# Performance work log

Measured on AMD Instinct MI355X. Metric: run time of the kernel, lower is better.

The kernel has to match this reference:

```python
import jax, jax.numpy as jnp
import numpy as np

BETA = 0.5
ITEM_NUM = 100000
REGION_NUM = 1000
EMBED = 128
HIDDEN = 256
B, H = 1024, 256


def setup_inputs() -> dict:
    key = jax.random.key(0)
    ks = jax.random.split(key, 10)
    history = jax.random.randint(ks[0], (B, H), 0, ITEM_NUM)
    target = jax.random.randint(ks[1], (B,), 0, ITEM_NUM)
    history_region = jax.random.randint(ks[2], (B, H), 0, REGION_NUM)
    target_region = jax.random.randint(ks[3], (B,), 0, REGION_NUM)
    E_hist = 0.01 * jax.random.normal(ks[4], (ITEM_NUM, EMBED), dtype=jnp.float32)
    E_targ = 0.01 * jax.random.normal(ks[5], (ITEM_NUM, EMBED), dtype=jnp.float32)
    E_reg = 0.01 * jax.random.normal(ks[6], (REGION_NUM, EMBED), dtype=jnp.float32)
    lim1 = 1.0 / np.sqrt(2 * EMBED)
    W1 = jax.random.uniform(ks[7], (2 * EMBED, HIDDEN), jnp.float32, -lim1, lim1)
    b1 = jnp.zeros((HIDDEN,), jnp.float32)
    lim2 = 1.0 / np.sqrt(HIDDEN)
    w2 = jax.random.uniform(ks[8], (HIDDEN,), jnp.float32, -lim2, lim2)
    return {"history": history, "target": target,
            "history_region": history_region, "target_region": target_region,
            "E_hist": E_hist, "E_targ": E_targ, "E_reg": E_reg,
            "W1": W1, "b1": b1, "w2": w2}


def reference(history, target, history_region, target_region,
              E_hist, E_targ, E_reg, W1, b1, w2):
    # gathers + concat: hist [B,H,2d], tgt [B,2d]
    hist = jnp.concatenate([E_hist[history], E_reg[history_region]], axis=-1)
    tgt = jnp.concatenate([E_targ[target], E_reg[target_region]], axis=-1)
    # elementwise product broadcast over history dim
    inp = hist * tgt[:, None, :]                      # [B,H,2d]
    hid = jax.nn.relu(jnp.einsum('bhd,dk->bhk', inp, W1) + b1)
    scores = jnp.einsum('bhk,k->bh', hid, w2)         # [B,H]
    mask = (history != target[:, None]).astype(scores.dtype)
    exp_a = jnp.exp(scores) * mask                    # [B,H]
    denom = jnp.power(jnp.sum(exp_a, axis=-1), BETA)  # [B]
    attn = exp_a / denom[:, None]                     # [B,H]
    # weighted reduction: sum_h sum_d hist*attn*tgt
    pred = jnp.einsum('bhd,bh,bd->b', hist, attn, tgt)
    return jax.nn.sigmoid(pred)
```

## Files before the change

### kernel.cpp

```cpp
#include <hip/hip_runtime.h>
#include <hip/hip_bf16.h>

#define NB 1024
#define NH 256
#define EMB 128
#define TWOD 256
#define HID 256
#define ROWS 128
#define BPB 2
#define NBLK (NB * BPB)

typedef __attribute__((ext_vector_type(4))) float f32x4;
typedef __attribute__((ext_vector_type(8))) short bf16x8;

__device__ __forceinline__ unsigned short f2bf(float f) {
  union { float f; unsigned u; } v; v.f = f;
  unsigned u = v.u;
  unsigned r = (u + 0x7fffu + ((u >> 16) & 1u)) >> 16;
  return (unsigned short)r;
}

__global__ __launch_bounds__(256) void prep_w1t(const float* __restrict__ W1,
                                                unsigned short* __restrict__ W1T) {
  const int bx = blockIdx.x & 3;
  const int by = blockIdx.x >> 2;
  __shared__ float tile[64][65];
  const int tr = threadIdx.x >> 6;
  const int tc = threadIdx.x & 63;
  #pragma unroll
  for (int i = 0; i < 16; ++i) {
    const int d = bx * 64 + i * 4 + tr;
    tile[i * 4 + tr][tc] = W1[(size_t)d * HID + by * 64 + tc];
  }
  __syncthreads();
  #pragma unroll
  for (int i = 0; i < 16; ++i) {
    const int n = by * 64 + i * 4 + tr;
    W1T[(size_t)n * TWOD + bx * 64 + tc] = f2bf(tile[tc][i * 4 + tr]);
  }
}

__global__ __launch_bounds__(512, 4) void nais_main(
    const int* __restrict__ history, const int* __restrict__ target,
    const int* __restrict__ hregion, const int* __restrict__ tregion,
    const float* __restrict__ E_hist, const float* __restrict__ E_targ,
    const float* __restrict__ E_reg,
    const unsigned short* __restrict__ W1T, const float* __restrict__ b1,
    const float* __restrict__ w2,
    float* __restrict__ part_se, float* __restrict__ part_sd)
{
  const int blk = blockIdx.x;
  const int b = blk >> 1;
  const int r0 = (blk & 1) * ROWS;
  const int tid = threadIdx.x;
  const int lane = tid & 63;
  const int wave = tid >> 6;
  const int l15 = lane & 15;
  const int lhi = lane >> 4;
  const int l31 = lane & 31;
  const int halfsel = lane >> 5;

  __shared__ __align__(16) unsigned short inp_lds[ROWS * 256];
  __shared__ float dot_lds[ROWS];
  __shared__ int items_lds[ROWS];
  __shared__ float score_parts[8][ROWS];

  const float* tsrc = halfsel ? (E_reg + (size_t)tregion[b] * EMB)
                              : (E_targ + (size_t)target[b] * EMB);
  const f32x4 t = *(const f32x4*)(tsrc + l31 * 4);
  const int tgt_item = target[b];

  const int* keysrc = halfsel ? hregion : history;
  const float* table = halfsel ? E_reg : E_hist;

  {
    int key[16];
    #pragma unroll
    for (int s = 0; s < 16; ++s)
      key[s] = keysrc[b * NH + r0 + wave * 16 + s];

    #pragma unroll
    for (int pass = 0; pass < 2; ++pass) {
      f32x4 vb[8];
      #pragma unroll
      for (int s = 0; s < 8; ++s)
        vb[s] = *(const f32x4*)(table + (size_t)key[pass * 8 + s] * EMB + l31 * 4);

      #pragma unroll
      for (int s = 0; s < 8; ++s) {
        const int row = wave * 16 + pass * 8 + s;
        if (lane == 0) items_lds[row] = key[pass * 8 + s];
        f32x4 v = vb[s] * t;
        float ds = v[0] + v[1] + v[2] + v[3];
        ds += __shfl_xor(ds, 1);
        ds += __shfl_xor(ds, 2);
        ds += __shfl_xor(ds, 4);
        ds += __shfl_xor(ds, 8);
        ds += __shfl_xor(ds, 16);
        ds += __shfl_xor(ds, 32);
        if (lane == 0) dot_lds[row] = ds;

        float2 f01; f01.x = v[0]; f01.y = v[1];
        float2 f23; f23.x = v[2]; f23.y = v[3];
        __hip_bfloat162 p0 = __float22bfloat162_rn(f01);
        __hip_bfloat162 p1 = __float22bfloat162_rn(f23);
        union { __hip_bfloat162 h; unsigned u; } c0, c1;
        c0.h = p0; c1.h = p1;
        const int g = halfsel * 16 + (l31 >> 1);
        const int gs = g ^ (row & 7) ^ ((g >> 3) & 3);
        unsigned* dst = (unsigned*)&inp_lds[row * 256 + gs * 8 + (lane & 1) * 4];
        dst[0] = c0.u; dst[1] = c1.u;
      }
    }
  }
  __syncthreads();

  {
    const int col0 = wave * 32;
    float b1v[2], w2v[2];
    #pragma unroll
    for (int n = 0; n < 2; ++n) {
      const int colh = col0 + n * 16 + l15;
      b1v[n] = b1[colh];
      w2v[n] = w2[colh];
    }

    f32x4 acc[2][4][2];
    #pragma unroll
    for (int c = 0; c < 2; ++c)
      #pragma unroll
      for (int m = 0; m < 4; ++m)
        #pragma unroll
        for (int n = 0; n < 2; ++n)
          acc[c][m][n] = (f32x4){0.f, 0.f, 0.f, 0.f};

    #pragma unroll
    for (int kk = 0; kk < 8; ++kk) {
      bf16x8 bfr[2];
      #pragma unroll
      for (int n = 0; n < 2; ++n) {
        const int colh = col0 + n * 16 + l15;
        bfr[n] = *(const bf16x8*)(W1T + (size_t)colh * TWOD + kk * 32 + lhi * 8);
      }
      bf16x8 af[2][4];
      #pragma unroll
      for (int c = 0; c < 2; ++c)
        #pragma unroll
        for (int m = 0; m < 4; ++m) {
          const int row = c * 64 + m * 16 + l15;
          const int gk = kk * 4 + lhi;
          const int gs = gk ^ (row & 7) ^ ((gk >> 3) & 3);
          af[c][m] = *(const bf16x8*)(&inp_lds[row * 256 + gs * 8]);
        }
      __builtin_amdgcn_s_setprio(1);
      #pragma unroll
      for (int c = 0; c < 2; ++c)
        #pragma unroll
        for (int m = 0; m < 4; ++m)
          #pragma unroll
          for (int n = 0; n < 2; ++n)
            acc[c][m][n] = __builtin_amdgcn_mfma_f32_16x16x32_bf16(af[c][m], bfr[n], acc[c][m][n], 0, 0, 0);
      __builtin_amdgcn_s_setprio(0);
    }

    #pragma unroll
    for (int c = 0; c < 2; ++c) {
      #pragma unroll
      for (int m = 0; m < 4; ++m) {
        #pragma unroll
        for (int r = 0; r < 4; ++r) {
          float p = 0.f;
          #pragma unroll
          for (int n = 0; n < 2; ++n) {
            float hv = acc[c][m][n][r] + b1v[n];
            hv = hv > 0.f ? hv : 0.f;
            p += hv * w2v[n];
          }
          p += __shfl_xor(p, 1);
          p += __shfl_xor(p, 2);
          p += __shfl_xor(p, 4);
          p += __shfl_xor(p, 8);
          if (l15 == 0) score_parts[wave][c * 64 + m * 16 + lhi * 4 + r] = p;
        }
      }
    }
  }
  __syncthreads();

  if (wave < 2) {
    const int lrow = wave * 64 + lane;
    float sc = 0.f;
    #pragma unroll
    for (int w = 0; w < 8; ++w) sc += score_parts[w][lrow];
    float e = (items_lds[lrow] != tgt_item) ? expf(sc) : 0.f;
    float ed = e * dot_lds[lrow];
    #pragma unroll
    for (int off = 32; off >= 1; off >>= 1) {
      e += __shfl_xor(e, off);
      ed += __shfl_xor(ed, off);
    }
    if (lane == 0) {
      part_se[blk * 2 + wave] = e;
      part_sd[blk * 2 + wave] = ed;
    }
  }
}

__global__ __launch_bounds__(256) void finalize(const float* __restrict__ part_se,
                                                const float* __restrict__ part_sd,
                                                float* __restrict__ out) {
  const int b = blockIdx.x * 256 + threadIdx.x;
  if (b < NB) {
    float se = 0.f, sd = 0.f;
    #pragma unroll
    for (int i = 0; i < BPB * 2; ++i) {
      se += part_se[b * BPB * 2 + i];
      sd += part_sd[b * BPB * 2 + i];
    }
    const float pred = (se > 0.f) ? (sd / sqrtf(se)) : 0.f;
    out[b] = 1.f / (1.f + expf(-pred));
  }
}

extern "C" void kernel_launch(void* const* d_in, const int* in_sizes, int n_in,
                              void* d_out, int out_size, void* d_ws, size_t ws_size,
                              hipStream_t stream) {
  const int* history = (const int*)d_in[0];
  const int* target  = (const int*)d_in[1];
  const int* hregion = (const int*)d_in[2];
  const int* tregion = (const int*)d_in[3];
  const float* E_hist = (const float*)d_in[4];
  const float* E_targ = (const float*)d_in[5];
  const float* E_reg  = (const float*)d_in[6];
  const float* W1 = (const float*)d_in[7];
  const float* b1 = (const float*)d_in[8];
  const float* w2 = (const float*)d_in[9];
  float* out = (float*)d_out;

  char* p = (char*)d_ws;
  unsigned short* W1T = (unsigned short*)p;  p += (size_t)TWOD * HID * 2;
  float* part_se = (float*)p;                p += (size_t)NBLK * 2 * 4;
  float* part_sd = (float*)p;

  prep_w1t<<<16, 256, 0, stream>>>(W1, W1T);
  nais_main<<<NBLK, 512, 0, stream>>>(history, target, hregion, tregion,
                                      E_hist, E_targ, E_reg, W1T, b1, w2,
                                      part_se, part_sd);
  finalize<<<(NB + 255) / 256, 256, 0, stream>>>(part_se, part_sd, out);
}
```

Baseline: 87.48 us.

## Warp-specialize producer/consumer waves with double-buffered chunks, one block per batch row

Each block now handles a whole batch row in four 64-row chunks. Four waves gather embeddings into a double-buffered LDS tile while the other four run the MFMA GEMM on the previous chunk, so gather latency overlaps with compute. The softmax-style reduction and sigmoid are folded into the main kernel, which removes the partial-sum buffers and the finalize launch. In exchange only half the waves do MFMA work, and a block barrier is needed at every chunk step.

```diff
diff --git a/kernel.cpp b/kernel.cpp
--- a/kernel.cpp
+++ b/kernel.cpp
@@ -6,9 +6,8 @@
 #define EMB 128
 #define TWOD 256
 #define HID 256
-#define ROWS 128
-#define BPB 2
-#define NBLK (NB * BPB)
+#define CR 64
+#define NCH 4
 
 typedef __attribute__((ext_vector_type(4))) float f32x4;
 typedef __attribute__((ext_vector_type(8))) short bf16x8;
@@ -46,12 +45,9 @@
     const float* __restrict__ E_hist, const float* __restrict__ E_targ,
     const float* __restrict__ E_reg,
     const unsigned short* __restrict__ W1T, const float* __restrict__ b1,
-    const float* __restrict__ w2,
-    float* __restrict__ part_se, float* __restrict__ part_sd)
+    const float* __restrict__ w2, float* __restrict__ out)
 {
-  const int blk = blockIdx.x;
-  const int b = blk >> 1;
-  const int r0 = (blk & 1) * ROWS;
+  const int b = blockIdx.x;
   const int tid = threadIdx.x;
   const int lane = tid & 63;
   const int wave = tid >> 6;
@@ -60,36 +56,48 @@
   const int l31 = lane & 31;
   const int halfsel = lane >> 5;
 
-  __shared__ __align__(16) unsigned short inp_lds[ROWS * 256];
-  __shared__ float dot_lds[ROWS];
-  __shared__ int items_lds[ROWS];
-  __shared__ float score_parts[8][ROWS];
-
-  const float* tsrc = halfsel ? (E_reg + (size_t)tregion[b] * EMB)
-                              : (E_targ + (size_t)target[b] * EMB);
-  const f32x4 t = *(const f32x4*)(tsrc + l31 * 4);
+  __shared__ __align__(16) unsigned short inp[2][CR * 256];
+  __shared__ float score_parts[2][4][CR];
+  __shared__ float dot_lds[NCH][CR];
+  __shared__ int items_lds[NCH][CR];
+
   const int tgt_item = target[b];
 
-  const int* keysrc = halfsel ? hregion : history;
-  const float* table = halfsel ? E_reg : E_hist;
-
-  {
+  f32x4 t;
+  const int* keysrc = history;
+  const float* table = E_hist;
+  float b1v[4], w2v[4];
+
+  if (wave < 4) {
+    const float* tsrc = halfsel ? (E_reg + (size_t)tregion[b] * EMB)
+                                : (E_targ + (size_t)target[b] * EMB);
+    t = *(const f32x4*)(tsrc + l31 * 4);
+    keysrc = halfsel ? hregion : history;
+    table = halfsel ? E_reg : E_hist;
+  } else {
+    const int col0 = (wave - 4) * 64;
+    #pragma unroll
+    for (int n = 0; n < 4; ++n) {
+      b1v[n] = b1[col0 + n * 16 + l15];
+      w2v[n] = w2[col0 + n * 16 + l15];
+    }
+  }
+
+  auto FILL = [&](int c, int buf) {
     int key[16];
     #pragma unroll
     for (int s = 0; s < 16; ++s)
-      key[s] = keysrc[b * NH + r0 + wave * 16 + s];
-
+      key[s] = keysrc[b * NH + c * CR + wave * 16 + s];
     #pragma unroll
     for (int pass = 0; pass < 2; ++pass) {
       f32x4 vb[8];
       #pragma unroll
       for (int s = 0; s < 8; ++s)
         vb[s] = *(const f32x4*)(table + (size_t)key[pass * 8 + s] * EMB + l31 * 4);
-
       #pragma unroll
       for (int s = 0; s < 8; ++s) {
         const int row = wave * 16 + pass * 8 + s;
-        if (lane == 0) items_lds[row] = key[pass * 8 + s];
+        if (lane == 0) items_lds[c][row] = key[pass * 8 + s];
         f32x4 v = vb[s] * t;
         float ds = v[0] + v[1] + v[2] + v[3];
         ds += __shfl_xor(ds, 1);
@@ -98,127 +106,110 @@
         ds += __shfl_xor(ds, 8);
         ds += __shfl_xor(ds, 16);
         ds += __shfl_xor(ds, 32);
-        if (lane == 0) dot_lds[row] = ds;
-
+        if (lane == 0) dot_lds[c][row] = ds;
         float2 f01; f01.x = v[0]; f01.y = v[1];
         float2 f23; f23.x = v[2]; f23.y = v[3];
-        __hip_bfloat162 p0 = __float22bfloat162_rn(f01);
-        __hip_bfloat162 p1 = __float22bfloat162_rn(f23);
         union { __hip_bfloat162 h; unsigned u; } c0, c1;
-        c0.h = p0; c1.h = p1;
+        c0.h = __float22bfloat162_rn(f01);
+        c1.h = __float22bfloat162_rn(f23);
         const int g = halfsel * 16 + (l31 >> 1);
         const int gs = g ^ (row & 7) ^ ((g >> 3) & 3);
-        unsigned* dst = (unsigned*)&inp_lds[row * 256 + gs * 8 + (lane & 1) * 4];
+        unsigned* dst = (unsigned*)&inp[buf][row * 256 + gs * 8 + (lane & 1) * 4];
         dst[0] = c0.u; dst[1] = c1.u;
       }
     }
-  }
-  __syncthreads();
-
-  {
-    const int col0 = wave * 32;
-    float b1v[2], w2v[2];
-    #pragma unroll
-    for (int n = 0; n < 2; ++n) {
-      const int colh = col0 + n * 16 + l15;
-      b1v[n] = b1[colh];
-      w2v[n] = w2[colh];
-    }
-
-    f32x4 acc[2][4][2];
-    #pragma unroll
-    for (int c = 0; c < 2; ++c)
+  };
+
+  float acc_e = 0.f, acc_ed = 0.f;
+
+  auto P3 = [&](int c) {
+    const int par = c & 1;
+    const float sc = score_parts[par][0][lane] + score_parts[par][1][lane] +
+                     score_parts[par][2][lane] + score_parts[par][3][lane];
+    const float e = (items_lds[c][lane] != tgt_item) ? expf(sc) : 0.f;
+    acc_e += e;
+    acc_ed += e * dot_lds[c][lane];
+  };
+
+  auto GEMM = [&](int c, int buf) {
+    const int col0 = (wave - 4) * 64;
+    f32x4 acc[4][4];
+    #pragma unroll
+    for (int m = 0; m < 4; ++m)
+      #pragma unroll
+      for (int n = 0; n < 4; ++n)
+        acc[m][n] = (f32x4){0.f, 0.f, 0.f, 0.f};
+
+    #pragma unroll
+    for (int kk = 0; kk < 8; ++kk) {
+      bf16x8 bfr[4];
+      #pragma unroll
+      for (int n = 0; n < 4; ++n)
+        bfr[n] = *(const bf16x8*)(W1T + (size_t)(col0 + n * 16 + l15) * TWOD + kk * 32 + lhi * 8);
+      bf16x8 af[4];
+      #pragma unroll
+      for (int m = 0; m < 4; ++m) {
+        const int row = m * 16 + l15;
+        const int gk = kk * 4 + lhi;
+        const int gs = gk ^ (row & 7) ^ ((gk >> 3) & 3);
+        af[m] = *(const bf16x8*)(&inp[buf][row * 256 + gs * 8]);
+      }
+      __builtin_amdgcn_s_setprio(1);
       #pragma unroll
       for (int m = 0; m < 4; ++m)
         #pragma unroll
-        for (int n = 0; n < 2; ++n)
-          acc[c][m][n] = (f32x4){0.f, 0.f, 0.f, 0.f};
-
-    #pragma unroll
-    for (int kk = 0; kk < 8; ++kk) {
-      bf16x8 bfr[2];
-      #pragma unroll
-      for (int n = 0; n < 2; ++n) {
-        const int colh = col0 + n * 16 + l15;
-        bfr[n] = *(const bf16x8*)(W1T + (size_t)colh * TWOD + kk * 32 + lhi * 8);
+        for (int n = 0; n < 4; ++n)
+          acc[m][n] = __builtin_amdgcn_mfma_f32_16x16x32_bf16(af[m], bfr[n], acc[m][n], 0, 0, 0);
+      __builtin_amdgcn_s_setprio(0);
+    }
+
+    const int cw = wave - 4;
+    #pragma unroll
+    for (int m = 0; m < 4; ++m) {
+      #pragma unroll
+      for (int r = 0; r < 4; ++r) {
+        float p = 0.f;
+        #pragma unroll
+        for (int n = 0; n < 4; ++n) {
+          float hv = acc[m][n][r] + b1v[n];
+          hv = hv > 0.f ? hv : 0.f;
+          p += hv * w2v[n];
+        }
+        p += __shfl_xor(p, 1);
+        p += __shfl_xor(p, 2);
+        p += __shfl_xor(p, 4);
+        p += __shfl_xor(p, 8);
+        if (l15 == 0) score_parts[c & 1][cw][m * 16 + lhi * 4 + r] = p;
       }
-      bf16x8 af[2][4];
-      #pragma unroll
-      for (int c = 0; c < 2; ++c)
-        #pragma unroll
-        for (int m = 0; m < 4; ++m) {
-          const int row = c * 64 + m * 16 + l15;
-          const int gk = kk * 4 + lhi;
-          const int gs = gk ^ (row & 7) ^ ((gk >> 3) & 3);
-          af[c][m] = *(const bf16x8*)(&inp_lds[row * 256 + gs * 8]);
-        }
-      __builtin_amdgcn_s_setprio(1);
-      #pragma unroll
-      for (int c = 0; c < 2; ++c)
-        #pragma unroll
-        for (int m = 0; m < 4; ++m)
-          #pragma unroll
-          for (int n = 0; n < 2; ++n)
-            acc[c][m][n] = __builtin_amdgcn_mfma_f32_16x16x32_bf16(af[c][m], bfr[n], acc[c][m][n], 0, 0, 0);
-      __builtin_amdgcn_s_setprio(0);
-    }
-
-    #pragma unroll
-    for (int c = 0; c < 2; ++c) {
-      #pragma unroll
-      for (int m = 0; m < 4; ++m) {
-        #pragma unroll
-        for (int r = 0; r < 4; ++r) {
-          float p = 0.f;
-          #pragma unroll
-          for (int n = 0; n < 2; ++n) {
-            float hv = acc[c][m][n][r] + b1v[n];
-            hv = hv > 0.f ? hv : 0.f;
-            p += hv * w2v[n];
-          }
-          p += __shfl_xor(p, 1);
-          p += __shfl_xor(p, 2);
-          p += __shfl_xor(p, 4);
-          p += __shfl_xor(p, 8);
-          if (l15 == 0) score_parts[wave][c * 64 + m * 16 + lhi * 4 + r] = p;
-        }
-      }
-    }
-  }
+    }
+  };
+
+  if (wave < 4) FILL(0, 0);
   __syncthreads();
 
-  if (wave < 2) {
-    const int lrow = wave * 64 + lane;
-    float sc = 0.f;
-    #pragma unroll
-    for (int w = 0; w < 8; ++w) sc += score_parts[w][lrow];
-    float e = (items_lds[lrow] != tgt_item) ? expf(sc) : 0.f;
-    float ed = e * dot_lds[lrow];
+  #pragma unroll
+  for (int tt = 0; tt < NCH; ++tt) {
+    if (wave < 4) {
+      if (tt < NCH - 1) FILL(tt + 1, (tt + 1) & 1);
+      if (wave == 0 && tt >= 1) P3(tt - 1);
+    } else {
+      GEMM(tt, tt & 1);
+    }
+    __syncthreads();
+  }
+
+  if (wave == 0) {
+    P3(NCH - 1);
+    float se = acc_e, sd = acc_ed;
     #pragma unroll
     for (int off = 32; off >= 1; off >>= 1) {
-      e += __shfl_xor(e, off);
-      ed += __shfl_xor(ed, off);
+      se += __shfl_xor(se, off);
+      sd += __shfl_xor(sd, off);
     }
     if (lane == 0) {
-      part_se[blk * 2 + wave] = e;
-      part_sd[blk * 2 + wave] = ed;
-    }
-  }
-}
-
-__global__ __launch_bounds__(256) void finalize(const float* __restrict__ part_se,
-                                                const float* __restrict__ part_sd,
-                                                float* __restrict__ out) {
-  const int b = blockIdx.x * 256 + threadIdx.x;
-  if (b < NB) {
-    float se = 0.f, sd = 0.f;
-    #pragma unroll
-    for (int i = 0; i < BPB * 2; ++i) {
-      se += part_se[b * BPB * 2 + i];
-      sd += part_sd[b * BPB * 2 + i];
-    }
-    const float pred = (se > 0.f) ? (sd / sqrtf(se)) : 0.f;
-    out[b] = 1.f / (1.f + expf(-pred));
+      const float pred = (se > 0.f) ? (sd / sqrtf(se)) : 0.f;
+      out[b] = 1.f / (1.f + expf(-pred));
+    }
   }
 }
 
@@ -237,14 +228,9 @@
   const float* w2 = (const float*)d_in[9];
   float* out = (float*)d_out;
 
-  char* p = (char*)d_ws;
-  unsigned short* W1T = (unsigned short*)p;  p += (size_t)TWOD * HID * 2;
-  float* part_se = (float*)p;                p += (size_t)NBLK * 2 * 4;
-  float* part_sd = (float*)p;
+  unsigned short* W1T = (unsigned short*)d_ws;
 
   prep_w1t<<<16, 256, 0, stream>>>(W1, W1T);
-  nais_main<<<NBLK, 512, 0, stream>>>(history, target, hregion, tregion,
-                                      E_hist, E_targ, E_reg, W1T, b1, w2,
-                                      part_se, part_sd);
-  finalize<<<(NB + 255) / 256, 256, 0, stream>>>(part_se, part_sd, out);
-}
+  nais_main<<<NB, 512, 0, stream>>>(history, target, hregion, tregion,
+                                    E_hist, E_targ, E_reg, W1T, b1, w2, out);
+}
```

Result: slower. 126.1 us (+44.2%).

## Split each batch row into four 64-row blocks with 4 waves each

Applied to the files above, without the earlier changes.

Halves rows per block (64 instead of 128) and threads per block (256 instead of 512), so four blocks cover each batch row. Each wave now computes 64 hidden columns over all 64 rows (4x4 MFMA tiles) instead of 32 columns over 128 rows. The score reduction and partial-sum layout shrink to match. LDS per block halves, which may allow more resident blocks. Each block now reloads the same W1T slice, so total W1T reads from L2 double.

```diff
diff --git a/kernel.cpp b/kernel.cpp
--- a/kernel.cpp
+++ b/kernel.cpp
@@ -6,8 +6,8 @@
 #define EMB 128
 #define TWOD 256
 #define HID 256
-#define ROWS 128
-#define BPB 2
+#define ROWS 64
+#define BPB 4
 #define NBLK (NB * BPB)
 
 typedef __attribute__((ext_vector_type(4))) float f32x4;
@@ -40,7 +40,7 @@
   }
 }
 
-__global__ __launch_bounds__(512, 4) void nais_main(
+__global__ __launch_bounds__(256, 4) void nais_main(
     const int* __restrict__ history, const int* __restrict__ target,
     const int* __restrict__ hregion, const int* __restrict__ tregion,
     const float* __restrict__ E_hist, const float* __restrict__ E_targ,
@@ -50,8 +50,8 @@
     float* __restrict__ part_se, float* __restrict__ part_sd)
 {
   const int blk = blockIdx.x;
-  const int b = blk >> 1;
-  const int r0 = (blk & 1) * ROWS;
+  const int b = blk >> 2;
+  const int r0 = (blk & 3) * ROWS;
   const int tid = threadIdx.x;
   const int lane = tid & 63;
   const int wave = tid >> 6;
@@ -63,7 +63,7 @@
   __shared__ __align__(16) unsigned short inp_lds[ROWS * 256];
   __shared__ float dot_lds[ROWS];
   __shared__ int items_lds[ROWS];
-  __shared__ float score_parts[8][ROWS];
+  __shared__ float score_parts[4][ROWS];
 
   const float* tsrc = halfsel ? (E_reg + (size_t)tregion[b] * EMB)
                               : (E_targ + (size_t)target[b] * EMB);
@@ -116,92 +116,81 @@
   __syncthreads();
 
   {
-    const int col0 = wave * 32;
-    float b1v[2], w2v[2];
-    #pragma unroll
-    for (int n = 0; n < 2; ++n) {
+    const int col0 = wave * 64;
+    float b1v[4], w2v[4];
+    #pragma unroll
+    for (int n = 0; n < 4; ++n) {
       const int colh = col0 + n * 16 + l15;
       b1v[n] = b1[colh];
       w2v[n] = w2[colh];
     }
 
-    f32x4 acc[2][4][2];
-    #pragma unroll
-    for (int c = 0; c < 2; ++c)
+    f32x4 acc[4][4];
+    #pragma unroll
+    for (int m = 0; m < 4; ++m)
+      #pragma unroll
+      for (int n = 0; n < 4; ++n)
+        acc[m][n] = (f32x4){0.f, 0.f, 0.f, 0.f};
+
+    #pragma unroll
+    for (int kk = 0; kk < 8; ++kk) {
+      bf16x8 bfr[4];
+      #pragma unroll
+      for (int n = 0; n < 4; ++n) {
+        const int colh = col0 + n * 16 + l15;
+        bfr[n] = *(const bf16x8*)(W1T + (size_t)colh * TWOD + kk * 32 + lhi * 8);
+      }
+      bf16x8 af[4];
+      #pragma unroll
+      for (int m = 0; m < 4; ++m) {
+        const int row = m * 16 + l15;
+        const int gk = kk * 4 + lhi;
+        const int gs = gk ^ (row & 7) ^ ((gk >> 3) & 3);
+        af[m] = *(const bf16x8*)(&inp_lds[row * 256 + gs * 8]);
+      }
+      __builtin_amdgcn_s_setprio(1);
       #pragma unroll
       for (int m = 0; m < 4; ++m)
         #pragma unroll
-        for (int n = 0; n < 2; ++n)
-          acc[c][m][n] = (f32x4){0.f, 0.f, 0.f, 0.f};
-
-    #pragma unroll
-    for (int kk = 0; kk < 8; ++kk) {
-      bf16x8 bfr[2];
-      #pragma unroll
-      for (int n = 0; n < 2; ++n) {
-        const int colh = col0 + n * 16 + l15;
-        bfr[n] = *(const bf16x8*)(W1T + (size_t)colh * TWOD + kk * 32 + lhi * 8);
-      }
-      bf16x8 af[2][4];
-      #pragma unroll
-      for (int c = 0; c < 2; ++c)
+        for (int n = 0; n < 4; ++n)
+          acc[m][n] = __builtin_amdgcn_mfma_f32_16x16x32_bf16(af[m], bfr[n], acc[m][n], 0, 0, 0);
+      __builtin_amdgcn_s_setprio(0);
+    }
+
+    #pragma unroll
+    for (int m = 0; m < 4; ++m) {
+      #pragma unroll
+      for (int r = 0; r < 4; ++r) {
+        float p = 0.f;
         #pragma unroll
-        for (int m = 0; m < 4; ++m) {
-          const int row = c * 64 + m * 16 + l15;
-          const int gk = kk * 4 + lhi;
-          const int gs = gk ^ (row & 7) ^ ((gk >> 3) & 3);
-          af[c][m] = *(const bf16x8*)(&inp_lds[row * 256 + gs * 8]);
+        for (int n = 0; n < 4; ++n) {
+          float hv = acc[m][n][r] + b1v[n];
+          hv = hv > 0.f ? hv : 0.f;
+          p += hv * w2v[n];
         }
-      __builtin_amdgcn_s_setprio(1);
-      #pragma unroll
-      for (int c = 0; c < 2; ++c)
-        #pragma unroll
-        for (int m = 0; m < 4; ++m)
-          #pragma unroll
-          for (int n = 0; n < 2; ++n)
-            acc[c][m][n] = __builtin_amdgcn_mfma_f32_16x16x32_bf16(af[c][m], bfr[n], acc[c][m][n], 0, 0, 0);
-      __builtin_amdgcn_s_setprio(0);
-    }
-
-    #pragma unroll
-    for (int c = 0; c < 2; ++c) {
-      #pragma unroll
-      for (int m = 0; m < 4; ++m) {
-        #pragma unroll
-        for (int r = 0; r < 4; ++r) {
-          float p = 0.f;
-          #pragma unroll
-          for (int n = 0; n < 2; ++n) {
-            float hv = acc[c][m][n][r] + b1v[n];
-            hv = hv > 0.f ? hv : 0.f;
-            p += hv * w2v[n];
-          }
-          p += __shfl_xor(p, 1);
-          p += __shfl_xor(p, 2);
-          p += __shfl_xor(p, 4);
-          p += __shfl_xor(p, 8);
-          if (l15 == 0) score_parts[wave][c * 64 + m * 16 + lhi * 4 + r] = p;
-        }
+        p += __shfl_xor(p, 1);
+        p += __shfl_xor(p, 2);
+        p += __shfl_xor(p, 4);
+        p += __shfl_xor(p, 8);
+        if (l15 == 0) score_parts[wave][m * 16 + lhi * 4 + r] = p;
       }
     }
   }
   __syncthreads();
 
-  if (wave < 2) {
-    const int lrow = wave * 64 + lane;
-    float sc = 0.f;
-    #pragma unroll
-    for (int w = 0; w < 8; ++w) sc += score_parts[w][lrow];
-    float e = (items_lds[lrow] != tgt_item) ? expf(sc) : 0.f;
-    float ed = e * dot_lds[lrow];
+  if (wave == 0) {
+    float sc = score_parts[0][lane] + score_parts[1][lane] +
+               score_parts[2][lane] + score_parts[3][lane];
+    float e = (items_lds[lane] != tgt_item) ? expf(sc) : 0.f;
+    float ed = e * dot_lds[lane];
     #pragma unroll
     for (int off = 32; off >= 1; off >>= 1) {
       e += __shfl_xor(e, off);
       ed += __shfl_xor(ed, off);
     }
     if (lane == 0) {
-      part_se[blk * 2 + wave] = e;
-      part_sd[blk * 2 + wave] = ed;
+      part_se[blk] = e;
+      part_sd[blk] = ed;
     }
   }
 }
@@ -213,9 +202,9 @@
   if (b < NB) {
     float se = 0.f, sd = 0.f;
     #pragma unroll
-    for (int i = 0; i < BPB * 2; ++i) {
-      se += part_se[b * BPB * 2 + i];
-      sd += part_sd[b * BPB * 2 + i];
+    for (int i = 0; i < BPB; ++i) {
+      se += part_se[b * BPB + i];
+      sd += part_sd[b * BPB + i];
     }
     const float pred = (se > 0.f) ? (sd / sqrtf(se)) : 0.f;
     out[b] = 1.f / (1.f + expf(-pred));
@@ -239,11 +228,11 @@
 
   char* p = (char*)d_ws;
   unsigned short* W1T = (unsigned short*)p;  p += (size_t)TWOD * HID * 2;
-  float* part_se = (float*)p;                p += (size_t)NBLK * 2 * 4;
+  float* part_se = (float*)p;                p += (size_t)NBLK * 4;
   float* part_sd = (float*)p;
 
   prep_w1t<<<16, 256, 0, stream>>>(W1, W1T);
-  nais_main<<<NBLK, 512, 0, stream>>>(history, target, hregion, tregion,
+  nais_main<<<NBLK, 256, 0, stream>>>(history, target, hregion, tregion,
                                       E_hist, E_targ, E_reg, W1T, b1, w2,
                                       part_se, part_sd);
   finalize<<<(NB + 255) / 256, 256, 0, stream>>>(part_se, part_sd, out);
```

Result: slower. 113.9 us (+30.2%).
